# Optimization experiments

Measured on AMD Instinct MI355X. Metric: run time of the kernel, lower is better.

## Reference

```python
import jax, jax.numpy as jnp
import numpy as np

N_EXPERTS = 8
TOP_K = 2


def setup_inputs() -> dict:
    key = jax.random.key(0)
    k1, k2, k3, k4 = jax.random.split(key, 4)
    B, T, C, H, E = 2, 2048, 1024, 4096, N_EXPERTS
    x = jax.random.normal(k1, (B, T, C), dtype=jnp.float32)
    # weights scaled like standard init to keep activations well-behaved
    router_w = jax.random.normal(k2, (E, C), dtype=jnp.float32) * 0.02
    w1 = jax.random.normal(k3, (E, C, H), dtype=jnp.float32) * (1.0 / np.sqrt(C))
    w2 = jax.random.normal(k4, (E, H, C), dtype=jnp.float32) * (1.0 / np.sqrt(H))
    return {"x": x, "router_w": router_w, "w1": w1, "w2": w2}


def reference(x, router_w, w1, w2):
    B, T, C = x.shape
    E = N_EXPERTS
    xf = x.reshape(-1, C)                                   # [N, C], N = B*T
    logits = jnp.einsum('nc,ec->ne', xf, router_w)          # router (no bias)
    probs = jax.nn.softmax(logits, axis=-1)
    top_w, top_i = jax.lax.top_k(probs, TOP_K)              # [N, K]
    top_w = top_w / jnp.sum(top_w, axis=-1, keepdims=True)  # renormalize
    # combine weight per (token, expert): sum of top-k weights routed to e
    comb = jnp.einsum('nk,nke->ne', top_w, jax.nn.one_hot(top_i, E, dtype=xf.dtype))
    # dense all-expert compute (bias=False, exact GELU, dropout=0 at eval)
    h = jax.nn.gelu(jnp.einsum('nc,ech->enh', xf, w1), approximate=False)  # [E, N, H]
    y = jnp.einsum('enh,ehc->enc', h, w2)                   # [E, N, C]
    out = jnp.einsum('ne,enc->nc', comb, y)                 # weighted combine
    return out.reshape(B, T, C)
```

## Files before the change

kernel.cpp:

```cpp
#include <hip/hip_runtime.h>
#include <hip/hip_bf16.h>
#include <stdint.h>

#define NTOK 4096
#define CD   1024
#define HD   4096
#define NE   8

typedef __attribute__((ext_vector_type(8))) short bf16x8;
typedef __attribute__((ext_vector_type(4))) float f32x4;
typedef __attribute__((ext_vector_type(4))) unsigned short us4;

__device__ __forceinline__ unsigned short f2bf(float f){
  __hip_bfloat16 h = __float2bfloat16(f);
  return *reinterpret_cast<unsigned short*>(&h);
}

__global__ __launch_bounds__(256) void router_kernel(
    const float* __restrict__ x, const float* __restrict__ rw,
    unsigned short* __restrict__ x_bf, int* __restrict__ top_i,
    float* __restrict__ top_w, int* __restrict__ counts){
  __shared__ float rw_lds[NE*CD];
  int tid = threadIdx.x;
  for (int i = tid; i < NE*CD/4; i += 256)
    ((float4*)rw_lds)[i] = ((const float4*)rw)[i];
  __syncthreads();
  int l = tid & 63, w = tid >> 6;
  int n = blockIdx.x*4 + w;

  float4 xv[4];
  #pragma unroll
  for (int j = 0; j < 4; ++j)
    xv[j] = ((const float4*)(x + (size_t)n*CD))[l + j*64];

  #pragma unroll
  for (int j = 0; j < 4; ++j){
    us4 o; o.x = f2bf(xv[j].x); o.y = f2bf(xv[j].y); o.z = f2bf(xv[j].z); o.w = f2bf(xv[j].w);
    *(us4*)(x_bf + (size_t)n*CD + l*4 + j*256) = o;
  }

  double le[NE];
  #pragma unroll
  for (int e = 0; e < NE; ++e){
    double p = 0.0;
    #pragma unroll
    for (int j = 0; j < 4; ++j){
      float4 rv = ((const float4*)(rw_lds + e*CD))[l + j*64];
      p += (double)xv[j].x*rv.x + (double)xv[j].y*rv.y + (double)xv[j].z*rv.z + (double)xv[j].w*rv.w;
    }
    #pragma unroll
    for (int d = 32; d >= 1; d >>= 1) p += __shfl_xor(p, d);
    le[e] = p;
  }
  if (l == 0){
    double m = le[0];
    #pragma unroll
    for (int e = 1; e < NE; ++e) m = le[e] > m ? le[e] : m;
    double pe[NE];
    #pragma unroll
    for (int e = 0; e < NE; ++e) pe[e] = exp(le[e]-m);
    int i0 = 0;
    #pragma unroll
    for (int e = 1; e < NE; ++e) if (pe[e] > pe[i0]) i0 = e;
    int i1 = (i0 == 0) ? 1 : 0;
    #pragma unroll
    for (int e = 0; e < NE; ++e){ if (e == i0) continue; if (pe[e] > pe[i1]) i1 = e; }
    double w0 = pe[i0], w1v = pe[i1], wsum = w0 + w1v;
    top_i[2*n] = i0; top_i[2*n+1] = i1;
    top_w[2*n] = (float)(w0/wsum); top_w[2*n+1] = (float)(w1v/wsum);
    atomicAdd(&counts[i0], 1); atomicAdd(&counts[i1], 1);
  }
}

__global__ void scan_kernel(const int* __restrict__ counts, int* __restrict__ offsets, int* __restrict__ cursor){
  if (threadIdx.x == 0){
    int s = 0;
    for (int e = 0; e < NE; ++e){ offsets[e] = s; cursor[e] = s; s += counts[e]; }
  }
}

__global__ __launch_bounds__(256) void scatter_kernel(
    const int* __restrict__ top_i, const float* __restrict__ top_w,
    int* __restrict__ cursor, int* __restrict__ g_tok, float* __restrict__ g_w){
  int n = blockIdx.x*256 + threadIdx.x;
  #pragma unroll
  for (int k = 0; k < 2; ++k){
    int e = top_i[2*n+k];
    int pos = atomicAdd(&cursor[e], 1);
    g_tok[pos] = n;
    g_w[pos] = top_w[2*n+k];
  }
}

template<int R, int S>
__global__ __launch_bounds__(256) void transpose_cvt(const float* __restrict__ in, unsigned short* __restrict__ outp){
  __shared__ float tile[64][65];
  int e = blockIdx.z;
  const float* ip = in + (size_t)e*R*S;
  unsigned short* op = outp + (size_t)e*R*S;
  int s0 = blockIdx.x*64, r0 = blockIdx.y*64;
  int tid = threadIdx.x;
  #pragma unroll
  for (int i = 0; i < 4; ++i){
    int lin = i*256 + tid;
    int rr = lin >> 4, c4 = lin & 15;
    float4 v = *(const float4*)(ip + (size_t)(r0+rr)*S + s0 + c4*4);
    tile[rr][c4*4+0] = v.x; tile[rr][c4*4+1] = v.y;
    tile[rr][c4*4+2] = v.z; tile[rr][c4*4+3] = v.w;
  }
  __syncthreads();
  #pragma unroll
  for (int i = 0; i < 4; ++i){
    int lin = i*256 + tid;
    int ss = lin >> 4, rq = lin & 15;
    us4 o;
    o.x = f2bf(tile[rq*4+0][ss]);
    o.y = f2bf(tile[rq*4+1][ss]);
    o.z = f2bf(tile[rq*4+2][ss]);
    o.w = f2bf(tile[rq*4+3][ss]);
    *(us4*)(op + (size_t)(s0+ss)*R + r0 + rq*4) = o;
  }
}

template<int KLEN, int SPLITK, int EPI>
__global__ __launch_bounds__(256, 4) void gemm2ph(
    const unsigned short* __restrict__ A_src,
    const unsigned short* __restrict__ B_src,
    unsigned short* __restrict__ h_out,
    float* __restrict__ outp,
    const int* __restrict__ g_tok,
    const float* __restrict__ g_w,
    const int* __restrict__ counts,
    const int* __restrict__ offsets,
    int NDIM, int KSTRIDE){
  constexpr int NT = KLEN/32;
  __shared__ alignas(128) char lds[32768];

  int z = blockIdx.z;
  int e  = (SPLITK == 1) ? z : (z / SPLITK);
  int kz = (SPLITK == 1) ? 0 : (z % SPLITK);
  int n_e = counts[e];
  int m0 = blockIdx.y*128;
  if (m0 >= n_e) return;
  int n0 = blockIdx.x*128;
  int g_base = offsets[e];
  int kstart = kz*KLEN;

  int tid = threadIdx.x, l = tid & 63, w = tid >> 6;
  int wr = w >> 1, wc = w & 1;
  int lrow = l & 15, q = l >> 4;

  const unsigned short* src[4];
  uint32_t dst[4];
  #pragma unroll
  for (int i = 0; i < 4; ++i){
    int g = i*256 + w*64 + l;
    bool isA = g < 512;
    int gg = isA ? g : (g - 512);
    int row = gg >> 2, c = gg & 3;
    int cs = c ^ (row & 3);
    if (isA){
      int rg = m0 + row; if (rg > n_e-1) rg = n_e-1;
      size_t arow;
      if (EPI == 0) arow = (size_t)g_tok[g_base + rg];
      else          arow = (size_t)(g_base + rg);
      src[i] = A_src + arow*(size_t)KSTRIDE + kstart + cs*8;
    } else {
      src[i] = B_src + ((size_t)e*NDIM + n0 + row)*(size_t)KSTRIDE + kstart + cs*8;
    }
    dst[i] = (uint32_t)g*16u;
  }

  uint32_t a_off[4], b_off[4];
  #pragma unroll
  for (int m = 0; m < 4; ++m){
    int ra = wr*64 + m*16 + lrow;
    a_off[m] = (uint32_t)(ra*64) + 16u*(q ^ (ra & 3));
    int rb = wc*64 + m*16 + lrow;
    b_off[m] = 8192u + (uint32_t)(rb*64) + 16u*(q ^ (rb & 3));
  }

  f32x4 acc[4][4] = {};

  #pragma unroll
  for (int i = 0; i < 4; ++i){
    __builtin_amdgcn_global_load_lds((const __attribute__((address_space(1))) void*)src[i],
                                     (__attribute__((address_space(3))) void*)&lds[dst[i]], 16, 0, 0);
    src[i] += 32;
  }
  __syncthreads();

  uint32_t buf = 0;
  #pragma unroll 1
  for (int kt = 0; kt < NT; ++kt){
    if (kt + 1 < NT){
      uint32_t nb = (buf ^ 1)*16384u;
      #pragma unroll
      for (int i = 0; i < 4; ++i){
        __builtin_amdgcn_global_load_lds((const __attribute__((address_space(1))) void*)src[i],
                                         (__attribute__((address_space(3))) void*)&lds[dst[i] + nb], 16, 0, 0);
        src[i] += 32;
      }
    }
    uint32_t ro = buf*16384u;
    bf16x8 av[4], bv[4];
    #pragma unroll
    for (int m = 0; m < 4; ++m){
      av[m] = *(const bf16x8*)&lds[a_off[m] + ro];
      bv[m] = *(const bf16x8*)&lds[b_off[m] + ro];
    }
    __builtin_amdgcn_s_setprio(1);
    #pragma unroll
    for (int m = 0; m < 4; ++m)
      #pragma unroll
      for (int n = 0; n < 4; ++n)
        acc[m][n] = __builtin_amdgcn_mfma_f32_16x16x32_bf16(av[m], bv[n], acc[m][n], 0, 0, 0);
    __builtin_amdgcn_s_setprio(0);
    __syncthreads();
    buf ^= 1;
  }

  if (EPI == 0){
    #pragma unroll
    for (int m = 0; m < 4; ++m){
      #pragma unroll
      for (int j = 0; j < 4; ++j){
        int r = m0 + wr*64 + m*16 + q*4 + j;
        if (r < n_e){
          unsigned short* hp = h_out + (size_t)(g_base + r)*NDIM + n0 + wc*64 + lrow;
          #pragma unroll
          for (int n = 0; n < 4; ++n){
            float v = acc[m][n][j];
            v = 0.5f*v*(1.0f + erff(v*0.70710678118654752f));
            hp[n*16] = f2bf(v);
          }
        }
      }
    }
  } else {
    #pragma unroll
    for (int m = 0; m < 4; ++m){
      #pragma unroll
      for (int j = 0; j < 4; ++j){
        int r = m0 + wr*64 + m*16 + q*4 + j;
        if (r < n_e){
          int slot = g_base + r;
          int t = g_tok[slot];
          float wgt = g_w[slot];
          float* op = outp + (size_t)t*NDIM + n0 + wc*64 + lrow;
          #pragma unroll
          for (int n = 0; n < 4; ++n)
            atomicAdd(op + n*16, wgt*acc[m][n][j]);
        }
      }
    }
  }
}

extern "C" void kernel_launch(void* const* d_in, const int* in_sizes, int n_in,
                              void* d_out, int out_size, void* d_ws, size_t ws_size,
                              hipStream_t stream) {
  const float* x  = (const float*)d_in[0];
  const float* rw = (const float*)d_in[1];
  const float* w1 = (const float*)d_in[2];
  const float* w2 = (const float*)d_in[3];

  size_t off = 0;
  auto alloc = [&](size_t sz) -> char* {
    char* p = (char*)d_ws + off;
    off += (sz + 255) & ~(size_t)255;
    return p;
  };
  unsigned short* x_bf = (unsigned short*)alloc((size_t)NTOK*CD*2);
  unsigned short* w1t  = (unsigned short*)alloc((size_t)NE*CD*HD*2);
  unsigned short* w2t  = (unsigned short*)alloc((size_t)NE*CD*HD*2);
  unsigned short* hbuf = (unsigned short*)alloc((size_t)NTOK*2*HD*2);
  int*   top_i  = (int*)alloc(NTOK*2*4);
  float* top_w  = (float*)alloc(NTOK*2*4);
  int*   counts = (int*)alloc(64);
  int*   offs   = (int*)alloc(64);
  int*   cursor = (int*)alloc(64);
  int*   g_tok  = (int*)alloc(NTOK*2*4);
  float* g_w    = (float*)alloc(NTOK*2*4);
  (void)ws_size; (void)in_sizes; (void)n_in; (void)out_size;

  hipMemsetAsync(d_out, 0, (size_t)NTOK*CD*4, stream);
  hipMemsetAsync(counts, 0, 64, stream);

  router_kernel<<<dim3(NTOK/4), dim3(256), 0, stream>>>(x, rw, x_bf, top_i, top_w, counts);
  scan_kernel<<<dim3(1), dim3(64), 0, stream>>>(counts, offs, cursor);
  scatter_kernel<<<dim3(NTOK/256), dim3(256), 0, stream>>>(top_i, top_w, cursor, g_tok, g_w);

  transpose_cvt<CD, HD><<<dim3(HD/64, CD/64, NE), dim3(256), 0, stream>>>(w1, w1t);
  transpose_cvt<HD, CD><<<dim3(CD/64, HD/64, NE), dim3(256), 0, stream>>>(w2, w2t);

  gemm2ph<CD, 1, 0><<<dim3(HD/128, 16, NE), dim3(256), 0, stream>>>(
      x_bf, w1t, hbuf, (float*)nullptr, g_tok, g_w, counts, offs, HD, CD);
  gemm2ph<HD/2, 2, 1><<<dim3(CD/128, 16, NE*2), dim3(256), 0, stream>>>(
      hbuf, w2t, (unsigned short*)nullptr, (float*)d_out, g_tok, g_w, counts, offs, CD, HD);
}
```

Before: 481.7 us.

## Replace double-buffered GEMM loop with 4-stage LDS ring and vmcnt waits

The expert GEMM kernels move from a two-buffer LDS pipeline to a four-slot ring. Three k-tiles are prefetched ahead using global_load_lds, and explicit s_waitcnt vmcnt counts plus a single s_barrier per iteration replace the trailing __syncthreads. This aims to hide global memory latency behind MFMA work and drop one barrier per k-step. In exchange LDS grows to 64KB, the occupancy hint falls from 4 to 2 blocks per CU, and correctness depends on the hand-written wait counts.

```diff
diff --git a/kernel.cpp b/kernel.cpp
--- a/kernel.cpp
+++ b/kernel.cpp
@@ -10,6 +10,11 @@
 typedef __attribute__((ext_vector_type(8))) short bf16x8;
 typedef __attribute__((ext_vector_type(4))) float f32x4;
 typedef __attribute__((ext_vector_type(4))) unsigned short us4;
+
+#define BARR() asm volatile("s_barrier" ::: "memory")
+#define VM8() asm volatile("s_waitcnt vmcnt(8)" ::: "memory")
+#define VM4() asm volatile("s_waitcnt vmcnt(4)" ::: "memory")
+#define VM0() asm volatile("s_waitcnt vmcnt(0)" ::: "memory")
 
 __device__ __forceinline__ unsigned short f2bf(float f){
   __hip_bfloat16 h = __float2bfloat16(f);
@@ -123,7 +128,7 @@
 }
 
 template<int KLEN, int SPLITK, int EPI>
-__global__ __launch_bounds__(256, 4) void gemm2ph(
+__global__ __launch_bounds__(256, 2) void gemm_ring(
     const unsigned short* __restrict__ A_src,
     const unsigned short* __restrict__ B_src,
     unsigned short* __restrict__ h_out,
@@ -134,7 +139,7 @@
     const int* __restrict__ offsets,
     int NDIM, int KSTRIDE){
   constexpr int NT = KLEN/32;
-  __shared__ alignas(128) char lds[32768];
+  __shared__ alignas(128) char lds[65536];
 
   int z = blockIdx.z;
   int e  = (SPLITK == 1) ? z : (z / SPLITK);
@@ -171,6 +176,15 @@
     dst[i] = (uint32_t)g*16u;
   }
 
+  auto STAGE = [&](int t){
+    uint32_t bb = (uint32_t)(t & 3)*16384u;
+    #pragma unroll
+    for (int i = 0; i < 4; ++i)
+      __builtin_amdgcn_global_load_lds(
+        (const __attribute__((address_space(1))) void*)(src[i] + (size_t)t*32),
+        (__attribute__((address_space(3))) void*)&lds[dst[i] + bb], 16, 0, 0);
+  };
+
   uint32_t a_off[4], b_off[4];
   #pragma unroll
   for (int m = 0; m < 4; ++m){
@@ -182,27 +196,16 @@
 
   f32x4 acc[4][4] = {};
 
-  #pragma unroll
-  for (int i = 0; i < 4; ++i){
-    __builtin_amdgcn_global_load_lds((const __attribute__((address_space(1))) void*)src[i],
-                                     (__attribute__((address_space(3))) void*)&lds[dst[i]], 16, 0, 0);
-    src[i] += 32;
-  }
-  __syncthreads();
-
-  uint32_t buf = 0;
+  STAGE(0); STAGE(1); STAGE(2);
+
   #pragma unroll 1
   for (int kt = 0; kt < NT; ++kt){
-    if (kt + 1 < NT){
-      uint32_t nb = (buf ^ 1)*16384u;
-      #pragma unroll
-      for (int i = 0; i < 4; ++i){
-        __builtin_amdgcn_global_load_lds((const __attribute__((address_space(1))) void*)src[i],
-                                         (__attribute__((address_space(3))) void*)&lds[dst[i] + nb], 16, 0, 0);
-        src[i] += 32;
-      }
-    }
-    uint32_t ro = buf*16384u;
+    if (kt < NT-2) { VM8(); }
+    else if (kt == NT-2) { VM4(); }
+    else { VM0(); }
+    BARR();
+    if (kt + 3 < NT) STAGE(kt + 3);
+    uint32_t ro = (uint32_t)(kt & 3)*16384u;
     bf16x8 av[4], bv[4];
     #pragma unroll
     for (int m = 0; m < 4; ++m){
@@ -216,8 +219,6 @@
       for (int n = 0; n < 4; ++n)
         acc[m][n] = __builtin_amdgcn_mfma_f32_16x16x32_bf16(av[m], bv[n], acc[m][n], 0, 0, 0);
     __builtin_amdgcn_s_setprio(0);
-    __syncthreads();
-    buf ^= 1;
   }
 
   if (EPI == 0){
@@ -294,8 +295,8 @@
   transpose_cvt<CD, HD><<<dim3(HD/64, CD/64, NE), dim3(256), 0, stream>>>(w1, w1t);
   transpose_cvt<HD, CD><<<dim3(CD/64, HD/64, NE), dim3(256), 0, stream>>>(w2, w2t);
 
-  gemm2ph<CD, 1, 0><<<dim3(HD/128, 16, NE), dim3(256), 0, stream>>>(
+  gemm_ring<CD, 1, 0><<<dim3(HD/128, 16, NE), dim3(256), 0, stream>>>(
       x_bf, w1t, hbuf, (float*)nullptr, g_tok, g_w, counts, offs, HD, CD);
-  gemm2ph<HD/2, 2, 1><<<dim3(CD/128, 16, NE*2), dim3(256), 0, stream>>>(
+  gemm_ring<HD/2, 2, 1><<<dim3(CD/128, 16, NE*2), dim3(256), 0, stream>>>(
       hbuf, w2t, (unsigned short*)nullptr, (float*)d_out, g_tok, g_w, counts, offs, CD, HD);
 }
```

Result: slower. 497.8 us (+3.3%).
